# Kernel optimization log

Measured on AMD Instinct MI355X. Metric: run time of the kernel, lower is better.

## Reference

```python
import jax, jax.numpy as jnp
import numpy as np

B, C, OC, H, W = 2, 64, 128, 96, 96
HD, DI, N, R, K = C // 2, C, 16, 2, 4  # VSSBlock: hidden=C/2, d_inner=2*hidden=C, d_state, dt_rank, 4 scan dirs
EPS = 1e-5


def _conv(x, w, b, pad, groups=1):
    y = jax.lax.conv_general_dilated(x, w, (1, 1), pad, feature_group_count=groups,
                                     dimension_numbers=('NCHW', 'OIHW', 'NCHW'))
    return y + b[None, :, None, None]


def _ln(x, w, b):
    m = x.mean(-1, keepdims=True)
    v = x.var(-1, keepdims=True)
    return (x - m) * jax.lax.rsqrt(v + EPS) * w + b


def _selective_scan(xs, dts, Bs, Cs, A, D):
    # xs, dts: (B,K,DI,L); Bs, Cs: (B,K,N,L); A: (K,DI,N); D: (K,DI)
    dts = jax.nn.softplus(dts)

    def step(h, inp):
        u_t, dt_t, B_t, C_t = inp
        dA = jnp.exp(dt_t[..., None] * A)                         # (B,K,DI,N)
        h = dA * h + (dt_t * u_t)[..., None] * B_t[:, :, None, :]
        return h, jnp.einsum('bkdn,bkn->bkd', h, C_t)

    seq = (jnp.moveaxis(xs, -1, 0), jnp.moveaxis(dts, -1, 0),
           jnp.moveaxis(Bs, -1, 0), jnp.moveaxis(Cs, -1, 0))
    h0 = jnp.zeros(xs.shape[:3] + (A.shape[-1],), xs.dtype)
    _, ys = jax.lax.scan(step, h0, seq)
    return jnp.moveaxis(ys, 0, -1) + D[None, :, :, None] * xs


def _vss_block(x, ln_w, ln_b, in_w, conv_w, conv_b, xproj_w, dtproj_w, dtproj_b,
               A_logs, Ds, on_w, on_b, out_w):
    # x: (B,H,W,HD); VMamba SS2D with 4-direction cross-scan + residual
    b, hh, ww, _ = x.shape
    L = hh * ww
    h = _ln(x, ln_w, ln_b)
    xz = h @ in_w                                   # (B,H,W,2*DI)
    xp, z = jnp.split(xz, 2, axis=-1)
    xc = jnp.transpose(xp, (0, 3, 1, 2))            # (B,DI,H,W)
    xc = jax.nn.silu(_conv(xc, conv_w, conv_b, ((1, 1), (1, 1)), groups=DI))
    x_flat = xc.reshape(b, DI, L)
    x_wh = jnp.transpose(xc, (0, 1, 3, 2)).reshape(b, DI, L)
    x2 = jnp.stack([x_flat, x_wh], axis=1)
    xs = jnp.concatenate([x2, jnp.flip(x2, -1)], axis=1)      # (B,4,DI,L)
    x_dbl = jnp.einsum('bkdl,kcd->bkcl', xs, xproj_w)
    dts, Bs, Cs = jnp.split(x_dbl, [R, R + N], axis=2)
    dts = jnp.einsum('bkrl,kdr->bkdl', dts, dtproj_w) + dtproj_b[None, :, :, None]
    A = -jnp.exp(A_logs)
    ys = _selective_scan(xs, dts, Bs, Cs, A, Ds)              # (B,4,DI,L)
    inv = jnp.flip(ys[:, 2:4], -1)
    unwh = lambda t: jnp.transpose(t.reshape(b, DI, ww, hh), (0, 1, 3, 2)).reshape(b, DI, L)
    y = ys[:, 0] + inv[:, 0] + unwh(ys[:, 1]) + unwh(inv[:, 1])
    y = jnp.transpose(y.reshape(b, DI, hh, ww), (0, 2, 3, 1))
    y = _ln(y, on_w, on_b) * jax.nn.silu(z)
    return x + y @ out_w


def _forward(x, ms_dw33_w, ms_dw33_b, ms_in_w, ms_in_b, ms_scale,
             vss_ln_w, vss_ln_b, vss_in_w, vss_conv_w, vss_conv_b, vss_xproj_w,
             vss_dtproj_w, vss_dtproj_b, vss_A_logs, vss_Ds, vss_on_w, vss_on_b, vss_out_w,
             ma_conv_w, ma_conv_b, adw_h_w, adw_h_b, adw_w_w, adw_w_b,
             pw_w, pw_b, bn_w, bn_b, bn_mean, bn_var):
    vss = (vss_ln_w, vss_ln_b, vss_in_w, vss_conv_w, vss_conv_b, vss_xproj_w,
           vss_dtproj_w, vss_dtproj_b, vss_A_logs, vss_Ds, vss_on_w, vss_on_b, vss_out_w)
    # --- MambaSplit (shared VSSBlock applied to both channel halves) ---
    xd = _conv(x, ms_dw33_w, ms_dw33_b, ((1, 1), (1, 1)), groups=C)
    x1, x2 = jnp.split(xd, 2, axis=1)

    def branch(xp):
        y = _vss_block(jnp.transpose(xp, (0, 2, 3, 1)), *vss)
        return ms_scale * xp + jnp.transpose(y, (0, 3, 1, 2))

    xm = jnp.concatenate([branch(x1), branch(x2)], axis=1)
    m = xm.mean((2, 3), keepdims=True)
    v = xm.var((2, 3), keepdims=True)
    xm = (xm - m) * jax.lax.rsqrt(v + EPS) * ms_in_w[None, :, None, None] + ms_in_b[None, :, None, None]
    xm = jax.nn.leaky_relu(xm, 0.01)
    # --- MaxAvg (global avg+max pool -> 3x3 conv on 1x1 map -> sigmoid gate) ---
    pooled = jnp.concatenate([x.mean((2, 3), keepdims=True), x.max((2, 3), keepdims=True)], axis=1)
    gate = jax.nn.sigmoid(_conv(pooled, ma_conv_w, ma_conv_b, ((1, 1), (1, 1))))
    xs_ = xm + gate * x
    # --- AxialDW ---
    xs_ = xs_ + _conv(xs_, adw_h_w, adw_h_b, ((1, 1), (0, 0)), groups=C) \
              + _conv(xs_, adw_w_w, adw_w_b, ((0, 0), (1, 1)), groups=C)
    # --- BN (eval) + ReLU, 1x1 conv, 2x2 maxpool ---
    skip = jax.nn.relu((xs_ - bn_mean[None, :, None, None]) * jax.lax.rsqrt(bn_var[None, :, None, None] + EPS)
                       * bn_w[None, :, None, None] + bn_b[None, :, None, None])
    out = _conv(skip, pw_w, pw_b, ((0, 0), (0, 0)))
    down = jax.lax.reduce_window(out, -jnp.inf, jax.lax.max, (1, 1, 2, 2), (1, 1, 2, 2), 'VALID')
    return down, skip


def setup_inputs() -> dict:
    key = jax.random.key(0)
    ks = jax.random.split(key, 16)
    r = lambda i, shape, s=0.02: jax.random.normal(ks[i], shape, jnp.float32) * s
    return {
        'x': jax.random.normal(ks[0], (B, C, H, W), jnp.float32),
        'ms_dw33_w': r(1, (C, 1, 3, 3), 0.1), 'ms_dw33_b': jnp.zeros(C),
        'ms_in_w': jnp.ones(C), 'ms_in_b': jnp.zeros(C),
        'ms_scale': jnp.ones((1,)),
        'vss_ln_w': jnp.ones(HD), 'vss_ln_b': jnp.zeros(HD),
        'vss_in_w': r(2, (HD, 2 * DI)),
        'vss_conv_w': r(3, (DI, 1, 3, 3), 0.1), 'vss_conv_b': jnp.zeros(DI),
        'vss_xproj_w': r(4, (K, R + 2 * N, DI)),
        'vss_dtproj_w': r(5, (K, DI, R), 0.1), 'vss_dtproj_b': r(6, (K, DI), 0.1),
        'vss_A_logs': jnp.tile(jnp.log(jnp.arange(1, N + 1, dtype=jnp.float32)), (K, DI, 1)),
        'vss_Ds': jnp.ones((K, DI)),
        'vss_on_w': jnp.ones(DI), 'vss_on_b': jnp.zeros(DI),
        'vss_out_w': r(7, (DI, HD)),
        'ma_conv_w': r(8, (C, 2 * C, 3, 3), 0.05), 'ma_conv_b': jnp.zeros(C),
        'adw_h_w': r(9, (C, 1, 3, 1), 0.1), 'adw_h_b': jnp.zeros(C),
        'adw_w_w': r(10, (C, 1, 1, 3), 0.1), 'adw_w_b': jnp.zeros(C),
        'pw_w': r(11, (OC, C, 1, 1)), 'pw_b': jnp.zeros(OC),
        'bn_w': jnp.ones(C), 'bn_b': jnp.zeros(C),
        'bn_mean': jnp.zeros(C), 'bn_var': jnp.ones(C),
    }


def reference(x, ms_dw33_w, ms_dw33_b, ms_in_w, ms_in_b, ms_scale,
              vss_ln_w, vss_ln_b, vss_in_w, vss_conv_w, vss_conv_b, vss_xproj_w,
              vss_dtproj_w, vss_dtproj_b, vss_A_logs, vss_Ds, vss_on_w, vss_on_b, vss_out_w,
              ma_conv_w, ma_conv_b, adw_h_w, adw_h_b, adw_w_w, adw_w_b,
              pw_w, pw_b, bn_w, bn_b, bn_mean, bn_var):
    return _forward(x, ms_dw33_w, ms_dw33_b, ms_in_w, ms_in_b, ms_scale,
                    vss_ln_w, vss_ln_b, vss_in_w, vss_conv_w, vss_conv_b, vss_xproj_w,
                    vss_dtproj_w, vss_dtproj_b, vss_A_logs, vss_Ds, vss_on_w, vss_on_b, vss_out_w,
                    ma_conv_w, ma_conv_b, adw_h_w, adw_h_b, adw_w_w, adw_w_b,
                    pw_w, pw_b, bn_w, bn_b, bn_mean, bn_var)
```

## Files before the change

### kernel.cpp

```cpp
#include <hip/hip_runtime.h>
#include <hip/hip_bf16.h>

typedef __hip_bfloat16 bf16;
#define DEV __device__ __forceinline__

constexpr int B_ = 2, C_ = 64, H_ = 96, W_ = 96, L_ = 9216;
constexpr int HD_ = 32, DI_ = 64, N_ = 16, K_ = 4, BB_ = 4;
constexpr int OC_ = 128;
constexpr int CH_ = 768, CL_ = 12;
constexpr int SEGN = 16, SEGC = 48;
constexpr float EPSF = 1e-5f;
constexpr int DOWN_SZ = B_ * OC_ * 48 * 48;

typedef __attribute__((ext_vector_type(8))) short short8;
typedef __attribute__((ext_vector_type(4))) float f32x4;

DEV float softplusf(float x) { return x > 15.f ? x : __logf(1.f + __expf(x)); }
DEV float b2f(bf16 v) { return __bfloat162float(v); }
DEV float lo16f(unsigned v) { return __uint_as_float(v << 16); }
DEV float hi16f(unsigned v) { return __uint_as_float(v & 0xffff0000u); }
DEV void unpk(uint4 a, uint4 b, float* v) {
  v[0] = lo16f(a.x); v[1] = hi16f(a.x); v[2] = lo16f(a.y); v[3] = hi16f(a.y);
  v[4] = lo16f(a.z); v[5] = hi16f(a.z); v[6] = lo16f(a.w); v[7] = hi16f(a.w);
  v[8] = lo16f(b.x); v[9] = hi16f(b.x); v[10] = lo16f(b.y); v[11] = hi16f(b.y);
  v[12] = lo16f(b.z); v[13] = hi16f(b.z); v[14] = lo16f(b.w); v[15] = hi16f(b.w);
}

__constant__ float kLogN[16] = {
  0.0f, 0.69314718f, 1.09861229f, 1.38629436f, 1.60943791f, 1.79175947f,
  1.94591015f, 2.07944154f, 2.19722458f, 2.30258509f, 2.39789527f,
  2.48490665f, 2.56494936f, 2.63905733f, 2.70805020f, 2.77258872f};

DEV void chunk_addr(int k, int chunk, int& idx0, int& stride) {
  int r8 = chunk & 7, q = chunk >> 3;
  if (k == 0)      { idx0 = chunk * CL_;                        stride = 1;   }
  else if (k == 1) { idx0 = (12 * r8) * 96 + q;                 stride = 96;  }
  else if (k == 2) { idx0 = L_ - 1 - chunk * CL_;               stride = -1;  }
  else             { idx0 = (95 - 12 * r8) * 96 + (95 - q);     stride = -96; }
}

DEV void pow_tree(float e1, float* ep) {
  float e2 = e1 * e1, e4 = e2 * e2, e8 = e4 * e4;
  float e3 = e2 * e1, e5 = e4 * e1, e6 = e4 * e2, e7 = e4 * e3;
  ep[0] = e1;  ep[1] = e2;  ep[2] = e3;  ep[3] = e4;
  ep[4] = e5;  ep[5] = e6;  ep[6] = e7;  ep[7] = e8;
  ep[8] = e8 * e1;  ep[9] = e8 * e2;  ep[10] = e8 * e3;  ep[11] = e8 * e4;
  ep[12] = e8 * e5; ep[13] = e8 * e6; ep[14] = e8 * e7;  ep[15] = e8 * e8;
}

DEV void ld_bu(const float* __restrict__ bB, const bf16* __restrict__ xcb, int d, int idx,
               uint4& qb0, uint4& qb1, float& t0, float& t1, float& u) {
  int uix = __builtin_amdgcn_readfirstlane(idx);
  const float* p = bB + (size_t)uix * 12;
  qb0 = *(const uint4*)p; qb1 = *(const uint4*)(p + 4);
  t0 = p[8]; t1 = p[9];
  u = b2f(xcb[(size_t)idx * DI_ + d]);
}
DEV void ld_bcu(const float* __restrict__ bB, const bf16* __restrict__ bC,
                const bf16* __restrict__ xcb, int d, int idx,
                uint4& qb0, uint4& qb1, uint4& qc0, uint4& qc1,
                float& t0, float& t1, float& u) {
  int uix = __builtin_amdgcn_readfirstlane(idx);
  const float* p = bB + (size_t)uix * 12;
  qb0 = *(const uint4*)p; qb1 = *(const uint4*)(p + 4);
  t0 = p[8]; t1 = p[9];
  const uint4* cq = (const uint4*)(bC + (size_t)uix * 16);
  qc0 = cq[0]; qc1 = cq[1];
  u = b2f(xcb[(size_t)idx * DI_ + d]);
}

__global__ void k_dw33(const float* __restrict__ x, const float* __restrict__ w,
                       const float* __restrict__ bias, float* __restrict__ out) {
  int t = blockIdx.x * 256 + threadIdx.x;
  if (t >= B_ * C_ * L_) return;
  int wi = t % W_, hi = (t / W_) % H_, c = (t / L_) % C_;
  float acc = bias[c];
#pragma unroll
  for (int dy = -1; dy <= 1; dy++) {
    int hh = hi + dy; if (hh < 0 || hh >= H_) continue;
#pragma unroll
    for (int dx = -1; dx <= 1; dx++) {
      int ww = wi + dx; if (ww < 0 || ww >= W_) continue;
      acc = fmaf(x[t + dy * W_ + dx], w[c * 9 + (dy + 1) * 3 + (dx + 1)], acc);
    }
  }
  out[t] = acc;
}

__global__ __launch_bounds__(256, 4) void k_ln_inproj(
    const float* __restrict__ xd, const float* __restrict__ lnw,
    const float* __restrict__ lnb, const float* __restrict__ inw,
    float* __restrict__ xzA, bf16* __restrict__ xzBh) {
  int bb = blockIdx.y, t = threadIdx.x;
  int b = bb & 1, co = (bb >> 1) * HD_;
  int idx0 = blockIdx.x * 64;
  __shared__ float xds[32 * 68];
  __shared__ float meanA[64], rstdA[64];
  int lane = t & 63;
  for (int r = 0; r < 8; r++) {
    int c = r * 4 + (t >> 6);
    xds[c * 68 + lane] = xd[(size_t)(b * C_ + co + c) * L_ + idx0 + lane];
  }
  __syncthreads();
  if (t < 64) {
    float s = 0.f, sq = 0.f;
#pragma unroll
    for (int c = 0; c < 32; c++) { float v = xds[c * 68 + t]; s += v; sq = fmaf(v, v, sq); }
    float mean = s * (1.f / HD_);
    float var = sq * (1.f / HD_) - mean * mean;
    meanA[t] = mean; rstdA[t] = rsqrtf(var + EPSF);
  }
  __syncthreads();
  for (int i = t; i < 2048; i += 256) {
    int c = i >> 6, idx = i & 63;
    float v = xds[c * 68 + idx];
    xds[c * 68 + idx] = (v - meanA[idx]) * rstdA[idx] * lnw[c] + lnb[c];
  }
  __syncthreads();
  int oc = t & 127, g = t >> 7;
  float acc[32];
#pragma unroll
  for (int j = 0; j < 32; j++) acc[j] = 0.f;
  for (int c = 0; c < 32; c++) {
    float wv = inw[c * 128 + oc];
    const float4* row = reinterpret_cast<const float4*>(&xds[c * 68 + g * 32]);
#pragma unroll
    for (int j4 = 0; j4 < 8; j4++) {
      float4 xv = row[j4];
      acc[j4 * 4 + 0] = fmaf(xv.x, wv, acc[j4 * 4 + 0]);
      acc[j4 * 4 + 1] = fmaf(xv.y, wv, acc[j4 * 4 + 1]);
      acc[j4 * 4 + 2] = fmaf(xv.z, wv, acc[j4 * 4 + 2]);
      acc[j4 * 4 + 3] = fmaf(xv.w, wv, acc[j4 * 4 + 3]);
    }
  }
  int occ = oc & 63;
  if (oc < 64) {
#pragma unroll
    for (int j = 0; j < 32; j++)
      xzA[(size_t)(bb * L_ + idx0 + g * 32 + j) * 64 + occ] = acc[j];
  } else {
#pragma unroll
    for (int j = 0; j < 32; j++)
      xzBh[(size_t)(bb * L_ + idx0 + g * 32 + j) * 64 + occ] = __float2bfloat16(acc[j]);
  }
}

__global__ void k_dwsilu(const float* __restrict__ xzA, const float* __restrict__ cw,
                         const float* __restrict__ cb, bf16* __restrict__ xch) {
  int t = blockIdx.x * 256 + threadIdx.x;
  int d = t & 63, idx = (t >> 6) % L_, bb = t / (L_ * DI_);
  int wi = idx % W_, hi = idx / W_;
  float acc = cb[d];
#pragma unroll
  for (int dy = -1; dy <= 1; dy++) {
    int hh = hi + dy; if (hh < 0 || hh >= H_) continue;
#pragma unroll
    for (int dx = -1; dx <= 1; dx++) {
      int ww = wi + dx; if (ww < 0 || ww >= W_) continue;
      acc = fmaf(xzA[(size_t)(bb * L_ + hh * W_ + ww) * 64 + d],
                 cw[d * 9 + (dy + 1) * 3 + (dx + 1)], acc);
    }
  }
  acc = acc / (1.f + __expf(-acc));
  xch[t] = __float2bfloat16(acc);
}

__global__ void k_wprep(const float* __restrict__ xpw, const float* __restrict__ alog,
                        bf16* __restrict__ wh, float* __restrict__ aux) {
  int i = blockIdx.x * 256 + threadIdx.x;
  if (i < 144 * 64) {
    int n = i >> 6;
    wh[i] = __float2bfloat16(n < 136 ? xpw[i] : 0.f);
  }
  if (blockIdx.x == 0 && threadIdx.x < 256) {
    int kd = threadIdx.x;
    const float* al = alog + kd * N_;
    float a0 = al[0];
    bool lin = true;
#pragma unroll
    for (int n = 1; n < N_; n++) lin = lin && (fabsf(al[n] - a0 - kLogN[n]) < 3e-5f);
    aux[kd] = -__expf(a0);
    aux[256 + kd] = lin ? 1.f : 0.f;
#pragma unroll
    for (int n = 0; n < N_; n++) aux[512 + kd * N_ + n] = -__expf(al[n]);
  }
}

__global__ __launch_bounds__(256, 4) void k_xdbl_mfma(
    const bf16* __restrict__ xch, const bf16* __restrict__ wh,
    float* __restrict__ xdblB, bf16* __restrict__ xdblC) {
  int w = threadIdx.x >> 6, lane = threadIdx.x & 63;
  int bb = blockIdx.y;
  int mtile = blockIdx.x * 4 + w;
  int idx0 = mtile * 16;
  int m = lane & 15, quad = lane >> 4;
  const bf16* arow = xch + ((size_t)bb * L_ + idx0 + m) * 64 + quad * 8;
  short8 a0 = *reinterpret_cast<const short8*>(arow);
  short8 a1 = *reinterpret_cast<const short8*>(arow + 32);
#pragma unroll
  for (int nt = 0; nt < 9; nt++) {
    int n = nt * 16 + m;
    const bf16* brow = wh + n * 64 + quad * 8;
    short8 b0 = *reinterpret_cast<const short8*>(brow);
    short8 b1 = *reinterpret_cast<const short8*>(brow + 32);
    f32x4 acc = {0.f, 0.f, 0.f, 0.f};
    acc = __builtin_amdgcn_mfma_f32_16x16x32_bf16(a0, b0, acc, 0, 0, 0);
    acc = __builtin_amdgcn_mfma_f32_16x16x32_bf16(a1, b1, acc, 0, 0, 0);
    if (n < 136) {
      int k4 = (n >= 102) ? 3 : (n >= 68) ? 2 : (n >= 34) ? 1 : 0;
      int c = n - k4 * 34;
      size_t row = (size_t)(bb * K_ + k4) * L_ + idx0 + quad * 4;
      if (c < 2) {
        float* db = xdblB + row * 12 + 8 + c;
        db[0] = acc[0]; db[12] = acc[1]; db[24] = acc[2]; db[36] = acc[3];
      } else if (c < 18) {
        bf16* bp = (bf16*)(xdblB + row * 12) + (c - 2);
        bp[0] = __float2bfloat16(acc[0]);  bp[24] = __float2bfloat16(acc[1]);
        bp[48] = __float2bfloat16(acc[2]); bp[72] = __float2bfloat16(acc[3]);
      } else {
        bf16* cp = xdblC + row * 16 + (c - 18);
        cp[0] = __float2bfloat16(acc[0]);  cp[16] = __float2bfloat16(acc[1]);
        cp[32] = __float2bfloat16(acc[2]); cp[48] = __float2bfloat16(acc[3]);
      }
    }
  }
}

__global__ __launch_bounds__(256, 4) void k_scan1(
    const float* __restrict__ xdblB, const bf16* __restrict__ xch,
    const float* __restrict__ dtw, const float* __restrict__ dtb,
    const float* __restrict__ aux, bf16* __restrict__ hbuf,
    float* __restrict__ ssum) {
  int w = threadIdx.x >> 6, d = threadIdx.x & 63;
  int chunk = blockIdx.x * 4 + w, k = blockIdx.y, bb = blockIdx.z;
  float w0 = dtw[(k * DI_ + d) * 2 + 0], w1 = dtw[(k * DI_ + d) * 2 + 1];
  float bia = dtb[k * DI_ + d];
  float A1 = aux[k * 64 + d];
  bool chain = (__ballot(aux[256 + k * 64 + d] > 0.5f) == ~0ull);
  float h[N_];
#pragma unroll
  for (int n = 0; n < N_; n++) h[n] = 0.f;
  int idx0, stride;
  chunk_addr(k, chunk, idx0, stride);
  const float* bB = xdblB + (size_t)(bb * K_ + k) * L_ * 12;
  const bf16* xcb = xch + (size_t)bb * L_ * DI_;
  float S = 0.f;
  if (chain) {
    int idx = idx0;
#pragma unroll 2
    for (int s = 0; s < CL_; s++) {
      uint4 qb0, qb1; float t0, t1, u;
      ld_bu(bB, xcb, d, idx, qb0, qb1, t0, t1, u);
      float Bv[16];
      unpk(qb0, qb1, Bv);
      float dt = softplusf(fmaf(t0, w0, fmaf(t1, w1, bia)));
      S += dt;
      float du = dt * u;
      float ep[16];
      pow_tree(__expf(dt * A1), ep);
#pragma unroll
      for (int n = 0; n < N_; n++) h[n] = fmaf(ep[n], h[n], du * Bv[n]);
      idx += stride;
    }
  } else {
    float A[N_];
#pragma unroll
    for (int n = 0; n < N_; n++) A[n] = aux[512 + (k * 64 + d) * N_ + n];
    int idx = idx0;
    for (int s = 0; s < CL_; s++) {
      uint4 qb0, qb1; float t0, t1, u;
      ld_bu(bB, xcb, d, idx, qb0, qb1, t0, t1, u);
      float Bv[16];
      unpk(qb0, qb1, Bv);
      float dt = softplusf(fmaf(t0, w0, fmaf(t1, w1, bia)));
      S += dt;
      float du = dt * u;
#pragma unroll
      for (int n = 0; n < N_; n++) h[n] = fmaf(__expf(dt * A[n]), h[n], du * Bv[n]);
      idx += stride;
    }
  }
  size_t base = (size_t)((bb * K_ + k) * CH_ + chunk) * DI_ + d;
  ssum[base] = S;
#pragma unroll
  for (int n = 0; n < N_; n++) hbuf[base * N_ + n] = __float2bfloat16(h[n]);
}

__global__ __launch_bounds__(256, 4) void k_scan2a(
    const float* __restrict__ aux, const float* __restrict__ ssum,
    bf16* __restrict__ hbuf, float* __restrict__ cumS,
    float* __restrict__ segH, float* __restrict__ segS) {
  int t = blockIdx.x * 256 + threadIdx.x;
  int n = t & 15, d = (t >> 4) & 63, kk = (t >> 10) & 3, bb = (t >> 12) & 3, seg = t >> 14;
  float A = aux[512 + (kk * 64 + d) * N_ + n];
  size_t row = (size_t)(bb * K_ + kk) * CH_ * DI_ + d;
  float hp = 0.f, Sc = 0.f;
#pragma unroll 4
  for (int j = 0; j < SEGC; j++) {
    int c = seg * SEGC + j;
    size_t sb = row + (size_t)c * DI_;
    float S = ssum[sb];
    float hl = b2f(hbuf[sb * N_ + n]);
    hbuf[sb * N_ + n] = __float2bfloat16(hp);
    if (n == 0) cumS[sb] = Sc;
    hp = fmaf(__expf(A * S), hp, hl);
    Sc += S;
  }
  size_t sbase = (size_t)(bb * K_ + kk) * SEGN + seg;
  segH[(sbase * DI_ + d) * N_ + n] = hp;
  if (n == 0) segS[sbase * DI_ + d] = Sc;
}

__global__ void k_scan2b(const float* __restrict__ aux, float* __restrict__ segH,
                         const float* __restrict__ segS) {
  int t = blockIdx.x * 256 + threadIdx.x;
  int n = t & 15, d = (t >> 4) & 63, kk = (t >> 10) & 3, bb = t >> 12;
  float A = aux[512 + (kk * 64 + d) * N_ + n];
  float hp = 0.f;
  for (int seg = 0; seg < SEGN; seg++) {
    size_t sbase = (size_t)(bb * K_ + kk) * SEGN + seg;
    size_t si = (sbase * DI_ + d) * N_ + n;
    float H = segH[si];
    float E = __expf(A * segS[sbase * DI_ + d]);
    segH[si] = hp;
    hp = fmaf(E, hp, H);
  }
}

__global__ __launch_bounds__(256, 4) void k_scan3(
    const float* __restrict__ xdblB, const bf16* __restrict__ xdblC,
    const bf16* __restrict__ xch, const float* __restrict__ dtw,
    const float* __restrict__ dtb, const float* __restrict__ Dsw,
    const float* __restrict__ aux, const bf16* __restrict__ hbuf,
    const float* __restrict__ cumS, const float* __restrict__ segH,
    bf16* __restrict__ ydir) {
  int w = threadIdx.x >> 6, d = threadIdx.x & 63;
  int chunk = blockIdx.x * 4 + w, k = blockIdx.y, bb = blockIdx.z;
  float w0 = dtw[(k * DI_ + d) * 2 + 0], w1 = dtw[(k * DI_ + d) * 2 + 1];
  float bia = dtb[k * DI_ + d];
  float Dk = Dsw[k * DI_ + d];
  float A1 = aux[k * 64 + d];
  bool chain = (__ballot(aux[256 + k * 64 + d] > 0.5f) == ~0ull);
  float h[N_];
  size_t base = (size_t)((bb * K_ + k) * CH_ + chunk) * DI_ + d;
  int seg = chunk / SEGC;
  size_t sbase = (size_t)(bb * K_ + k) * SEGN + seg;
  float Sc = cumS[base];
  {
    const bf16* hb = hbuf + base * N_;
    uint4 qh0 = *(const uint4*)hb, qh1 = *(const uint4*)(hb + 8);
    unpk(qh0, qh1, h);
    const float* Hin = segH + (sbase * DI_ + d) * N_;
    if (chain) {
      float ep[16];
      pow_tree(__expf(A1 * Sc), ep);
#pragma unroll
      for (int n = 0; n < N_; n++) h[n] = fmaf(ep[n], Hin[n], h[n]);
    } else {
#pragma unroll
      for (int n = 0; n < N_; n++) {
        float A = aux[512 + (k * 64 + d) * N_ + n];
        h[n] = fmaf(__expf(A * Sc), Hin[n], h[n]);
      }
    }
  }
  int idx0, stride;
  chunk_addr(k, chunk, idx0, stride);
  const float* bB = xdblB + (size_t)(bb * K_ + k) * L_ * 12;
  const bf16* bC = xdblC + (size_t)(bb * K_ + k) * L_ * 16;
  const bf16* xcb = xch + (size_t)bb * L_ * DI_;
  bf16* yb = ydir + (size_t)(bb * K_ + k) * L_ * DI_;
  if (chain) {
    int idx = idx0;
#pragma unroll 2
    for (int s = 0; s < CL_; s++) {
      uint4 qb0, qb1, qc0, qc1; float t0, t1, u;
      ld_bcu(bB, bC, xcb, d, idx, qb0, qb1, qc0, qc1, t0, t1, u);
      float Bv[16], Cv[16];
      unpk(qb0, qb1, Bv); unpk(qc0, qc1, Cv);
      float dt = softplusf(fmaf(t0, w0, fmaf(t1, w1, bia)));
      float du = dt * u;
      float ep[16];
      pow_tree(__expf(dt * A1), ep);
      float m[16];
#pragma unroll
      for (int n = 0; n < N_; n++) {
        h[n] = fmaf(ep[n], h[n], du * Bv[n]);
        m[n] = h[n] * Cv[n];
      }
      float a0 = m[0] + m[1], a1 = m[2] + m[3], a2 = m[4] + m[5], a3 = m[6] + m[7];
      float a4 = m[8] + m[9], a5 = m[10] + m[11], a6 = m[12] + m[13], a7 = m[14] + m[15];
      float b0 = a0 + a1, b1 = a2 + a3, b2 = a4 + a5, b3 = a6 + a7;
      float y = fmaf(Dk, u, (b0 + b1) + (b2 + b3));
      yb[(size_t)idx * DI_ + d] = __float2bfloat16(y);
      idx += stride;
    }
  } else {
    float A[N_];
#pragma unroll
    for (int n = 0; n < N_; n++) A[n] = aux[512 + (k * 64 + d) * N_ + n];
    int idx = idx0;
    for (int s = 0; s < CL_; s++) {
      uint4 qb0, qb1, qc0, qc1; float t0, t1, u;
      ld_bcu(bB, bC, xcb, d, idx, qb0, qb1, qc0, qc1, t0, t1, u);
      float Bv[16], Cv[16];
      unpk(qb0, qb1, Bv); unpk(qc0, qc1, Cv);
      float dt = softplusf(fmaf(t0, w0, fmaf(t1, w1, bia)));
      float du = dt * u;
      float y = 0.f;
#pragma unroll
      for (int n = 0; n < N_; n++) {
        h[n] = fmaf(__expf(dt * A[n]), h[n], du * Bv[n]);
        y = fmaf(h[n], Cv[n], y);
      }
      y = fmaf(Dk, u, y);
      yb[(size_t)idx * DI_ + d] = __float2bfloat16(y);
      idx += stride;
    }
  }
}

__global__ void k_combine(const bf16* __restrict__ ydir, const bf16* __restrict__ xzBh,
                          const float* __restrict__ xd, const float* __restrict__ onw,
                          const float* __restrict__ onb, const float* __restrict__ outw,
                          const float* __restrict__ mssc, float* __restrict__ xm) {
  int w = threadIdx.x >> 6, d = threadIdx.x & 63;
  int idx = blockIdx.x * 4 + w, bb = blockIdx.y;
  int b = bb & 1, co = (bb >> 1) * HD_;
  const bf16* yd = ydir + (size_t)bb * K_ * L_ * DI_;
  size_t off = (size_t)idx * DI_ + d;
  float y = b2f(yd[off]) + b2f(yd[(size_t)L_ * DI_ + off])
          + b2f(yd[(size_t)2 * L_ * DI_ + off]) + b2f(yd[(size_t)3 * L_ * DI_ + off]);
  float s = y, sq = y * y;
#pragma unroll
  for (int m = 1; m < 64; m <<= 1) { s += __shfl_xor(s, m, 64); sq += __shfl_xor(sq, m, 64); }
  float mean = s * (1.f / DI_);
  float var = sq * (1.f / DI_) - mean * mean;
  float rstd = rsqrtf(var + EPSF);
  float yn = (y - mean) * rstd * onw[d] + onb[d];
  float z = b2f(xzBh[(size_t)(bb * L_ + idx) * 64 + d]);
  float g = yn * (z / (1.f + __expf(-z)));
  __shared__ float gs[4][DI_];
  gs[w][d] = g;
  __syncthreads();
  if (d < HD_) {
    float acc = 0.f;
#pragma unroll
    for (int dd = 0; dd < DI_; dd++) acc = fmaf(gs[w][dd], outw[dd * HD_ + d], acc);
    size_t xi = (size_t)(b * C_ + co + d) * L_ + idx;
    float xp = xd[xi];
    xm[xi] = mssc[0] * xp + xp + acc;
  }
}

__global__ __launch_bounds__(1024) void k_stats(
    const float* __restrict__ xm, const float* __restrict__ x,
    float* __restrict__ inm, float* __restrict__ inr,
    float* __restrict__ xmean, float* __restrict__ xmax) {
  int bc = blockIdx.x, t = threadIdx.x;
  const float* pm = xm + (size_t)bc * L_;
  const float* px = x + (size_t)bc * L_;
  float s = 0.f, sq = 0.f, xs = 0.f, mx = -1e30f;
  for (int i = t; i < L_; i += 1024) {
    float v = pm[i]; s += v; sq = fmaf(v, v, sq);
    float xv = px[i]; xs += xv; mx = fmaxf(mx, xv);
  }
  __shared__ float red[64];
#pragma unroll
  for (int m = 1; m < 64; m <<= 1) {
    s += __shfl_xor(s, m, 64); sq += __shfl_xor(sq, m, 64);
    xs += __shfl_xor(xs, m, 64); mx = fmaxf(mx, __shfl_xor(mx, m, 64));
  }
  int wid = t >> 6;
  if ((t & 63) == 0) { red[wid] = s; red[16 + wid] = sq; red[32 + wid] = xs; red[48 + wid] = mx; }
  __syncthreads();
  if (t == 0) {
    s = 0.f; sq = 0.f; xs = 0.f; mx = -1e30f;
#pragma unroll
    for (int i = 0; i < 16; i++) {
      s += red[i]; sq += red[16 + i]; xs += red[32 + i]; mx = fmaxf(mx, red[48 + i]);
    }
    float mean = s * (1.f / L_);
    float var = sq * (1.f / L_) - mean * mean;
    inm[bc] = mean;
    inr[bc] = rsqrtf(var + EPSF);
    xmean[bc] = xs * (1.f / L_);
    xmax[bc] = mx;
  }
}

__global__ void k_xs(const float* __restrict__ xm, const float* __restrict__ inm,
                     const float* __restrict__ inr, const float* __restrict__ msw,
                     const float* __restrict__ msb, const float* __restrict__ xmean,
                     const float* __restrict__ xmax, const float* __restrict__ maw,
                     const float* __restrict__ mab, const float* __restrict__ x,
                     float* __restrict__ xs2) {
  int t = blockIdx.x * 256 + threadIdx.x;
  int bc = t / L_, c = bc & 63, b = bc >> 6;
  __shared__ float gsh;
  if (threadIdx.x < 64) {
    int ic = threadIdx.x;
    float p = xmean[b * 64 + ic] * maw[(c * 128 + ic) * 9 + 4]
            + xmax[b * 64 + ic] * maw[(c * 128 + 64 + ic) * 9 + 4];
#pragma unroll
    for (int m = 1; m < 64; m <<= 1) p += __shfl_xor(p, m, 64);
    if (ic == 0) gsh = 1.f / (1.f + __expf(-(p + mab[c])));
  }
  __syncthreads();
  float gate = gsh;
  float v = xm[t];
  v = (v - inm[bc]) * inr[bc] * msw[c] + msb[c];
  v = v > 0.f ? v : 0.01f * v;
  xs2[t] = v + gate * x[t];
}

__global__ void k_axbn(const float* __restrict__ xs2, const float* __restrict__ hw,
                       const float* __restrict__ hb, const float* __restrict__ wwt,
                       const float* __restrict__ wb, const float* __restrict__ bnw,
                       const float* __restrict__ bnb, const float* __restrict__ bnm,
                       const float* __restrict__ bnv, float* __restrict__ skipo) {
  int t = blockIdx.x * 256 + threadIdx.x;
  if (t >= B_ * C_ * L_) return;
  int wi = t % W_, hi = (t / W_) % H_, c = (t / L_) % C_;
  float a = xs2[t];
  float hacc = hb[c];
#pragma unroll
  for (int dy = -1; dy <= 1; dy++) {
    int hh = hi + dy; if (hh < 0 || hh >= H_) continue;
    hacc = fmaf(xs2[t + dy * W_], hw[c * 3 + dy + 1], hacc);
  }
  float wacc = wb[c];
#pragma unroll
  for (int dx = -1; dx <= 1; dx++) {
    int ww = wi + dx; if (ww < 0 || ww >= W_) continue;
    wacc = fmaf(xs2[t + dx], wwt[c * 3 + dx + 1], wacc);
  }
  float v = a + hacc + wacc;
  float sv = (v - bnm[c]) * rsqrtf(bnv[c] + EPSF) * bnw[c] + bnb[c];
  skipo[t] = fmaxf(sv, 0.f);
}

__global__ void k_pwpool(const float* __restrict__ skipo, const float* __restrict__ pww,
                         const float* __restrict__ pwb, float* __restrict__ down) {
  int h2 = blockIdx.x, b = blockIdx.y, t = threadIdx.x;
  int oc0 = blockIdx.z * 32;
  __shared__ float sk[64 * 192];
  for (int i = t; i < 64 * 192; i += 256) {
    int c = i / 192, rw = i % 192, r = rw / 96, wcol = rw % 96;
    sk[i] = skipo[((size_t)(b * C_ + c) * H_ + (2 * h2 + r)) * W_ + wcol];
  }
  __syncthreads();
  for (int o = t; o < 32 * 48; o += 256) {
    int oc = oc0 + o / 48, w2 = o % 48;
    float s0 = 0.f, s1 = 0.f, s2 = 0.f, s3 = 0.f;
#pragma unroll 8
    for (int c = 0; c < 64; c++) {
      float wv = pww[oc * 64 + c];
      const float* sp = &sk[c * 192 + 2 * w2];
      s0 = fmaf(sp[0], wv, s0);
      s1 = fmaf(sp[1], wv, s1);
      s2 = fmaf(sp[96], wv, s2);
      s3 = fmaf(sp[97], wv, s3);
    }
    float v = fmaxf(fmaxf(s0, s1), fmaxf(s2, s3)) + pwb[oc];
    down[((size_t)(b * OC_ + oc) * 48 + h2) * 48 + w2] = v;
  }
}

extern "C" void kernel_launch(void* const* d_in, const int* in_sizes, int n_in,
                              void* d_out, int out_size, void* d_ws, size_t ws_size,
                              hipStream_t stream) {
  const float* x     = (const float*)d_in[0];
  const float* dw33w = (const float*)d_in[1];
  const float* dw33b = (const float*)d_in[2];
  const float* msw   = (const float*)d_in[3];
  const float* msb   = (const float*)d_in[4];
  const float* mssc  = (const float*)d_in[5];
  const float* lnw   = (const float*)d_in[6];
  const float* lnb   = (const float*)d_in[7];
  const float* inw   = (const float*)d_in[8];
  const float* cw    = (const float*)d_in[9];
  const float* cb    = (const float*)d_in[10];
  const float* xpw   = (const float*)d_in[11];
  const float* dtw   = (const float*)d_in[12];
  const float* dtb   = (const float*)d_in[13];
  const float* alog  = (const float*)d_in[14];
  const float* Dsw   = (const float*)d_in[15];
  const float* onw   = (const float*)d_in[16];
  const float* onb   = (const float*)d_in[17];
  const float* outw  = (const float*)d_in[18];
  const float* maw   = (const float*)d_in[19];
  const float* mab   = (const float*)d_in[20];
  const float* ahw   = (const float*)d_in[21];
  const float* ahb   = (const float*)d_in[22];
  const float* aww   = (const float*)d_in[23];
  const float* awb   = (const float*)d_in[24];
  const float* pww   = (const float*)d_in[25];
  const float* pwb   = (const float*)d_in[26];
  const float* bnw   = (const float*)d_in[27];
  const float* bnb   = (const float*)d_in[28];
  const float* bnm   = (const float*)d_in[29];
  const float* bnv   = (const float*)d_in[30];

  float* ws = (float*)d_ws;
  float* xd    = ws;
  float* hreg  = xd + 1179648;
  bf16*  hbuf  = (bf16*)hreg;
  float* xzA   = hreg;
  bf16*  xzBh  = (bf16*)(hreg + 6291456);
  float* xdblB = hreg + 6291456 + 1179648;
  bf16*  xdblC = (bf16*)(xdblB + 1769472);
  float* ssum  = xdblB + 1769472 + 1179648;
  bf16*  ydir  = (bf16*)(ssum + 786432);
  float* xmR   = ssum + 786432 + 4718592;
  bf16*  xch   = (bf16*)xmR;
  float* xm    = xmR;
  float* xs2   = (float*)ydir;
  float* st    = xmR + 1179648;
  float* inm = st, *inr = st + 128, *xmean = st + 256, *xmaxv = st + 384;
  float* aux   = st + 512;
  bf16*  wh    = (bf16*)(aux + 4608);
  float* cumS  = aux + 4608 + 4608;
  float* segH  = cumS + 786432;
  float* segS  = segH + 262144;

  float* outp = (float*)d_out;
  float* down = outp;
  float* skipo = outp + DOWN_SZ;

  dim3 b256(256);
  int nEl = B_ * C_ * L_;

  k_wprep<<<dim3(36), b256, 0, stream>>>(xpw, alog, wh, aux);
  k_dw33<<<dim3((nEl + 255) / 256), b256, 0, stream>>>(x, dw33w, dw33b, xd);
  k_ln_inproj<<<dim3(L_ / 64, BB_), b256, 0, stream>>>(xd, lnw, lnb, inw, xzA, xzBh);
  k_dwsilu<<<dim3(BB_ * L_ * DI_ / 256), b256, 0, stream>>>(xzA, cw, cb, xch);
  k_xdbl_mfma<<<dim3(L_ / 64, BB_), b256, 0, stream>>>(xch, wh, xdblB, xdblC);
  k_scan1<<<dim3(CH_ / 4, K_, BB_), b256, 0, stream>>>(xdblB, xch, dtw, dtb, aux, hbuf, ssum);
  k_scan2a<<<dim3(BB_ * K_ * SEGN * DI_ * N_ / 256), b256, 0, stream>>>(aux, ssum, hbuf, cumS, segH, segS);
  k_scan2b<<<dim3(BB_ * K_ * DI_ * N_ / 256), b256, 0, stream>>>(aux, segH, segS);
  k_scan3<<<dim3(CH_ / 4, K_, BB_), b256, 0, stream>>>(xdblB, xdblC, xch, dtw, dtb, Dsw,
                                                      aux, hbuf, cumS, segH, ydir);
  k_combine<<<dim3(L_ / 4, BB_), b256, 0, stream>>>(ydir, xzBh, xd, onw, onb, outw, mssc, xm);
  k_stats<<<dim3(B_ * C_), dim3(1024), 0, stream>>>(xm, x, inm, inr, xmean, xmaxv);
  k_xs<<<dim3((nEl + 255) / 256), b256, 0, stream>>>(xm, inm, inr, msw, msb, xmean, xmaxv, maw, mab, x, xs2);
  k_axbn<<<dim3((nEl + 255) / 256), b256, 0, stream>>>(xs2, ahw, ahb, aww, awb, bnw, bnb, bnm, bnv, skipo);
  k_pwpool<<<dim3(48, B_, 4), b256, 0, stream>>>(skipo, pww, pwb, down);
}
```

Measured before the change: 321.0 us.

## Store scan inputs and outputs in per-direction scan order with a transposed copy

The depthwise SiLU kernel now also writes a transposed copy of its activations. The x_dbl projection writes B, C and dt rows in each direction's scan order, so both scan passes read and write contiguously instead of walking with stride 96 or -96. The combine kernel now undoes the per-direction permutation when it sums the four outputs. The cost is an extra activation buffer, scattered writes in the projection kernel, and strided gathers in combine.

```diff
diff --git a/kernel.cpp b/kernel.cpp
--- a/kernel.cpp
+++ b/kernel.cpp
@@ -31,14 +31,6 @@
   1.94591015f, 2.07944154f, 2.19722458f, 2.30258509f, 2.39789527f,
   2.48490665f, 2.56494936f, 2.63905733f, 2.70805020f, 2.77258872f};
 
-DEV void chunk_addr(int k, int chunk, int& idx0, int& stride) {
-  int r8 = chunk & 7, q = chunk >> 3;
-  if (k == 0)      { idx0 = chunk * CL_;                        stride = 1;   }
-  else if (k == 1) { idx0 = (12 * r8) * 96 + q;                 stride = 96;  }
-  else if (k == 2) { idx0 = L_ - 1 - chunk * CL_;               stride = -1;  }
-  else             { idx0 = (95 - 12 * r8) * 96 + (95 - q);     stride = -96; }
-}
-
 DEV void pow_tree(float e1, float* ep) {
   float e2 = e1 * e1, e4 = e2 * e2, e8 = e4 * e4;
   float e3 = e2 * e1, e5 = e4 * e1, e6 = e4 * e2, e7 = e4 * e3;
@@ -48,25 +40,25 @@
   ep[12] = e8 * e5; ep[13] = e8 * e6; ep[14] = e8 * e7;  ep[15] = e8 * e8;
 }
 
-DEV void ld_bu(const float* __restrict__ bB, const bf16* __restrict__ xcb, int d, int idx,
-               uint4& qb0, uint4& qb1, float& t0, float& t1, float& u) {
-  int uix = __builtin_amdgcn_readfirstlane(idx);
-  const float* p = bB + (size_t)uix * 12;
+DEV void ld_bu(const float* __restrict__ bB, const bf16* __restrict__ ub, int d,
+               int ls, int uidx, uint4& qb0, uint4& qb1, float& t0, float& t1, float& u) {
+  int uls = __builtin_amdgcn_readfirstlane(ls);
+  const float* p = bB + (size_t)uls * 12;
   qb0 = *(const uint4*)p; qb1 = *(const uint4*)(p + 4);
   t0 = p[8]; t1 = p[9];
-  u = b2f(xcb[(size_t)idx * DI_ + d]);
+  u = b2f(ub[(size_t)uidx * DI_ + d]);
 }
 DEV void ld_bcu(const float* __restrict__ bB, const bf16* __restrict__ bC,
-                const bf16* __restrict__ xcb, int d, int idx,
+                const bf16* __restrict__ ub, int d, int ls, int uidx,
                 uint4& qb0, uint4& qb1, uint4& qc0, uint4& qc1,
                 float& t0, float& t1, float& u) {
-  int uix = __builtin_amdgcn_readfirstlane(idx);
-  const float* p = bB + (size_t)uix * 12;
+  int uls = __builtin_amdgcn_readfirstlane(ls);
+  const float* p = bB + (size_t)uls * 12;
   qb0 = *(const uint4*)p; qb1 = *(const uint4*)(p + 4);
   t0 = p[8]; t1 = p[9];
-  const uint4* cq = (const uint4*)(bC + (size_t)uix * 16);
+  const uint4* cq = (const uint4*)(bC + (size_t)uls * 16);
   qc0 = cq[0]; qc1 = cq[1];
-  u = b2f(xcb[(size_t)idx * DI_ + d]);
+  u = b2f(ub[(size_t)uidx * DI_ + d]);
 }
 
 __global__ void k_dw33(const float* __restrict__ x, const float* __restrict__ w,
@@ -146,7 +138,8 @@
 }
 
 __global__ void k_dwsilu(const float* __restrict__ xzA, const float* __restrict__ cw,
-                         const float* __restrict__ cb, bf16* __restrict__ xch) {
+                         const float* __restrict__ cb, bf16* __restrict__ xch,
+                         bf16* __restrict__ xcht) {
   int t = blockIdx.x * 256 + threadIdx.x;
   int d = t & 63, idx = (t >> 6) % L_, bb = t / (L_ * DI_);
   int wi = idx % W_, hi = idx / W_;
@@ -162,7 +155,10 @@
     }
   }
   acc = acc / (1.f + __expf(-acc));
-  xch[t] = __float2bfloat16(acc);
+  bf16 v = __float2bfloat16(acc);
+  xch[t] = v;
+  int idx_t = wi * 96 + hi;
+  xcht[((size_t)bb * L_ + idx_t) * DI_ + d] = v;
 }
 
 __global__ void k_wprep(const float* __restrict__ xpw, const float* __restrict__ alog,
@@ -209,18 +205,16 @@
     if (n < 136) {
       int k4 = (n >= 102) ? 3 : (n >= 68) ? 2 : (n >= 34) ? 1 : 0;
       int c = n - k4 * 34;
-      size_t row = (size_t)(bb * K_ + k4) * L_ + idx0 + quad * 4;
-      if (c < 2) {
-        float* db = xdblB + row * 12 + 8 + c;
-        db[0] = acc[0]; db[12] = acc[1]; db[24] = acc[2]; db[36] = acc[3];
-      } else if (c < 18) {
-        bf16* bp = (bf16*)(xdblB + row * 12) + (c - 2);
-        bp[0] = __float2bfloat16(acc[0]);  bp[24] = __float2bfloat16(acc[1]);
-        bp[48] = __float2bfloat16(acc[2]); bp[72] = __float2bfloat16(acc[3]);
-      } else {
-        bf16* cp = xdblC + row * 16 + (c - 18);
-        cp[0] = __float2bfloat16(acc[0]);  cp[16] = __float2bfloat16(acc[1]);
-        cp[32] = __float2bfloat16(acc[2]); cp[48] = __float2bfloat16(acc[3]);
+#pragma unroll
+      for (int i = 0; i < 4; i++) {
+        int r = idx0 + quad * 4 + i;
+        int hi2 = r / 96, wi2 = r - hi2 * 96;
+        int tr = wi2 * 96 + hi2;
+        int ls = (k4 == 0) ? r : (k4 == 1) ? tr : (k4 == 2) ? (L_ - 1 - r) : (L_ - 1 - tr);
+        size_t row = (size_t)(bb * K_ + k4) * L_ + ls;
+        if (c < 2)       xdblB[row * 12 + 8 + c] = acc[i];
+        else if (c < 18) ((bf16*)(xdblB + row * 12))[c - 2] = __float2bfloat16(acc[i]);
+        else             xdblC[row * 16 + (c - 18)] = __float2bfloat16(acc[i]);
       }
     }
   }
@@ -228,9 +222,9 @@
 
 __global__ __launch_bounds__(256, 4) void k_scan1(
     const float* __restrict__ xdblB, const bf16* __restrict__ xch,
-    const float* __restrict__ dtw, const float* __restrict__ dtb,
-    const float* __restrict__ aux, bf16* __restrict__ hbuf,
-    float* __restrict__ ssum) {
+    const bf16* __restrict__ xcht, const float* __restrict__ dtw,
+    const float* __restrict__ dtb, const float* __restrict__ aux,
+    bf16* __restrict__ hbuf, float* __restrict__ ssum) {
   int w = threadIdx.x >> 6, d = threadIdx.x & 63;
   int chunk = blockIdx.x * 4 + w, k = blockIdx.y, bb = blockIdx.z;
   float w0 = dtw[(k * DI_ + d) * 2 + 0], w1 = dtw[(k * DI_ + d) * 2 + 1];
@@ -240,17 +234,17 @@
   float h[N_];
 #pragma unroll
   for (int n = 0; n < N_; n++) h[n] = 0.f;
-  int idx0, stride;
-  chunk_addr(k, chunk, idx0, stride);
   const float* bB = xdblB + (size_t)(bb * K_ + k) * L_ * 12;
-  const bf16* xcb = xch + (size_t)bb * L_ * DI_;
+  const bf16* ub = ((k & 1) ? xcht : xch) + (size_t)bb * L_ * DI_;
+  int ls0 = chunk * CL_;
+  int uidx0 = (k & 2) ? (L_ - 1 - ls0) : ls0;
+  int ustep = (k & 2) ? -1 : 1;
   float S = 0.f;
   if (chain) {
-    int idx = idx0;
 #pragma unroll 2
     for (int s = 0; s < CL_; s++) {
       uint4 qb0, qb1; float t0, t1, u;
-      ld_bu(bB, xcb, d, idx, qb0, qb1, t0, t1, u);
+      ld_bu(bB, ub, d, ls0 + s, uidx0 + s * ustep, qb0, qb1, t0, t1, u);
       float Bv[16];
       unpk(qb0, qb1, Bv);
       float dt = softplusf(fmaf(t0, w0, fmaf(t1, w1, bia)));
@@ -260,16 +254,14 @@
       pow_tree(__expf(dt * A1), ep);
 #pragma unroll
       for (int n = 0; n < N_; n++) h[n] = fmaf(ep[n], h[n], du * Bv[n]);
-      idx += stride;
     }
   } else {
     float A[N_];
 #pragma unroll
     for (int n = 0; n < N_; n++) A[n] = aux[512 + (k * 64 + d) * N_ + n];
-    int idx = idx0;
     for (int s = 0; s < CL_; s++) {
       uint4 qb0, qb1; float t0, t1, u;
-      ld_bu(bB, xcb, d, idx, qb0, qb1, t0, t1, u);
+      ld_bu(bB, ub, d, ls0 + s, uidx0 + s * ustep, qb0, qb1, t0, t1, u);
       float Bv[16];
       unpk(qb0, qb1, Bv);
       float dt = softplusf(fmaf(t0, w0, fmaf(t1, w1, bia)));
@@ -277,7 +269,6 @@
       float du = dt * u;
 #pragma unroll
       for (int n = 0; n < N_; n++) h[n] = fmaf(__expf(dt * A[n]), h[n], du * Bv[n]);
-      idx += stride;
     }
   }
   size_t base = (size_t)((bb * K_ + k) * CH_ + chunk) * DI_ + d;
@@ -329,11 +320,11 @@
 
 __global__ __launch_bounds__(256, 4) void k_scan3(
     const float* __restrict__ xdblB, const bf16* __restrict__ xdblC,
-    const bf16* __restrict__ xch, const float* __restrict__ dtw,
-    const float* __restrict__ dtb, const float* __restrict__ Dsw,
-    const float* __restrict__ aux, const bf16* __restrict__ hbuf,
-    const float* __restrict__ cumS, const float* __restrict__ segH,
-    bf16* __restrict__ ydir) {
+    const bf16* __restrict__ xch, const bf16* __restrict__ xcht,
+    const float* __restrict__ dtw, const float* __restrict__ dtb,
+    const float* __restrict__ Dsw, const float* __restrict__ aux,
+    const bf16* __restrict__ hbuf, const float* __restrict__ cumS,
+    const float* __restrict__ segH, bf16* __restrict__ ydir) {
   int w = threadIdx.x >> 6, d = threadIdx.x & 63;
   int chunk = blockIdx.x * 4 + w, k = blockIdx.y, bb = blockIdx.z;
   float w0 = dtw[(k * DI_ + d) * 2 + 0], w1 = dtw[(k * DI_ + d) * 2 + 1];
@@ -364,18 +355,18 @@
       }
     }
   }
-  int idx0, stride;
-  chunk_addr(k, chunk, idx0, stride);
   const float* bB = xdblB + (size_t)(bb * K_ + k) * L_ * 12;
   const bf16* bC = xdblC + (size_t)(bb * K_ + k) * L_ * 16;
-  const bf16* xcb = xch + (size_t)bb * L_ * DI_;
+  const bf16* ub = ((k & 1) ? xcht : xch) + (size_t)bb * L_ * DI_;
   bf16* yb = ydir + (size_t)(bb * K_ + k) * L_ * DI_;
+  int ls0 = chunk * CL_;
+  int uidx0 = (k & 2) ? (L_ - 1 - ls0) : ls0;
+  int ustep = (k & 2) ? -1 : 1;
   if (chain) {
-    int idx = idx0;
 #pragma unroll 2
     for (int s = 0; s < CL_; s++) {
       uint4 qb0, qb1, qc0, qc1; float t0, t1, u;
-      ld_bcu(bB, bC, xcb, d, idx, qb0, qb1, qc0, qc1, t0, t1, u);
+      ld_bcu(bB, bC, ub, d, ls0 + s, uidx0 + s * ustep, qb0, qb1, qc0, qc1, t0, t1, u);
       float Bv[16], Cv[16];
       unpk(qb0, qb1, Bv); unpk(qc0, qc1, Cv);
       float dt = softplusf(fmaf(t0, w0, fmaf(t1, w1, bia)));
@@ -392,17 +383,15 @@
       float a4 = m[8] + m[9], a5 = m[10] + m[11], a6 = m[12] + m[13], a7 = m[14] + m[15];
       float b0 = a0 + a1, b1 = a2 + a3, b2 = a4 + a5, b3 = a6 + a7;
       float y = fmaf(Dk, u, (b0 + b1) + (b2 + b3));
-      yb[(size_t)idx * DI_ + d] = __float2bfloat16(y);
-      idx += stride;
+      yb[(size_t)(ls0 + s) * DI_ + d] = __float2bfloat16(y);
     }
   } else {
     float A[N_];
 #pragma unroll
     for (int n = 0; n < N_; n++) A[n] = aux[512 + (k * 64 + d) * N_ + n];
-    int idx = idx0;
     for (int s = 0; s < CL_; s++) {
       uint4 qb0, qb1, qc0, qc1; float t0, t1, u;
-      ld_bcu(bB, bC, xcb, d, idx, qb0, qb1, qc0, qc1, t0, t1, u);
+      ld_bcu(bB, bC, ub, d, ls0 + s, uidx0 + s * ustep, qb0, qb1, qc0, qc1, t0, t1, u);
       float Bv[16], Cv[16];
       unpk(qb0, qb1, Bv); unpk(qc0, qc1, Cv);
       float dt = softplusf(fmaf(t0, w0, fmaf(t1, w1, bia)));
@@ -414,8 +403,7 @@
         y = fmaf(h[n], Cv[n], y);
       }
       y = fmaf(Dk, u, y);
-      yb[(size_t)idx * DI_ + d] = __float2bfloat16(y);
-      idx += stride;
+      yb[(size_t)(ls0 + s) * DI_ + d] = __float2bfloat16(y);
     }
   }
 }
@@ -427,10 +415,13 @@
   int w = threadIdx.x >> 6, d = threadIdx.x & 63;
   int idx = blockIdx.x * 4 + w, bb = blockIdx.y;
   int b = bb & 1, co = (bb >> 1) * HD_;
+  int hii = idx / 96, wii = idx - hii * 96;
+  int lt = wii * 96 + hii;
   const bf16* yd = ydir + (size_t)bb * K_ * L_ * DI_;
-  size_t off = (size_t)idx * DI_ + d;
-  float y = b2f(yd[off]) + b2f(yd[(size_t)L_ * DI_ + off])
-          + b2f(yd[(size_t)2 * L_ * DI_ + off]) + b2f(yd[(size_t)3 * L_ * DI_ + off]);
+  float y = b2f(yd[((size_t)0 * L_ + idx) * DI_ + d])
+          + b2f(yd[((size_t)1 * L_ + lt) * DI_ + d])
+          + b2f(yd[((size_t)2 * L_ + (L_ - 1 - idx)) * DI_ + d])
+          + b2f(yd[((size_t)3 * L_ + (L_ - 1 - lt)) * DI_ + d]);
   float s = y, sq = y * y;
 #pragma unroll
   for (int m = 1; m < 64; m <<= 1) { s += __shfl_xor(s, m, 64); sq += __shfl_xor(sq, m, 64); }
@@ -623,6 +614,7 @@
   float* cumS  = aux + 4608 + 4608;
   float* segH  = cumS + 786432;
   float* segS  = segH + 262144;
+  bf16*  xcht  = (bf16*)(segS + 16384);
 
   float* outp = (float*)d_out;
   float* down = outp;
@@ -634,12 +626,12 @@
   k_wprep<<<dim3(36), b256, 0, stream>>>(xpw, alog, wh, aux);
   k_dw33<<<dim3((nEl + 255) / 256), b256, 0, stream>>>(x, dw33w, dw33b, xd);
   k_ln_inproj<<<dim3(L_ / 64, BB_), b256, 0, stream>>>(xd, lnw, lnb, inw, xzA, xzBh);
-  k_dwsilu<<<dim3(BB_ * L_ * DI_ / 256), b256, 0, stream>>>(xzA, cw, cb, xch);
+  k_dwsilu<<<dim3(BB_ * L_ * DI_ / 256), b256, 0, stream>>>(xzA, cw, cb, xch, xcht);
   k_xdbl_mfma<<<dim3(L_ / 64, BB_), b256, 0, stream>>>(xch, wh, xdblB, xdblC);
-  k_scan1<<<dim3(CH_ / 4, K_, BB_), b256, 0, stream>>>(xdblB, xch, dtw, dtb, aux, hbuf, ssum);
+  k_scan1<<<dim3(CH_ / 4, K_, BB_), b256, 0, stream>>>(xdblB, xch, xcht, dtw, dtb, aux, hbuf, ssum);
   k_scan2a<<<dim3(BB_ * K_ * SEGN * DI_ * N_ / 256), b256, 0, stream>>>(aux, ssum, hbuf, cumS, segH, segS);
   k_scan2b<<<dim3(BB_ * K_ * DI_ * N_ / 256), b256, 0, stream>>>(aux, segH, segS);
-  k_scan3<<<dim3(CH_ / 4, K_, BB_), b256, 0, stream>>>(xdblB, xdblC, xch, dtw, dtb, Dsw,
+  k_scan3<<<dim3(CH_ / 4, K_, BB_), b256, 0, stream>>>(xdblB, xdblC, xch, xcht, dtw, dtb, Dsw,
                                                       aux, hbuf, cumS, segH, ydir);
   k_combine<<<dim3(L_ / 4, BB_), b256, 0, stream>>>(ydir, xzBh, xd, onw, onb, outw, mssc, xm);
   k_stats<<<dim3(B_ * C_), dim3(1024), 0, stream>>>(xm, x, inm, inr, xmean, xmaxv);
```

Result: no change. 320.7 us (-0.1%).
